# Performance work log

Measured on AMD Instinct MI355X. Metric: run time of the kernel, lower is better.

The kernel has to match this reference:

```python
import jax, jax.numpy as jnp
import numpy as np

B, S, D = 4, 2048, 1024
H, DH = 16, 64

def setup_inputs() -> dict:
    key = jax.random.key(0)
    kx, kq, kk, kv, ko = jax.random.split(key, 5)
    scale = 1.0 / np.sqrt(D)
    return {
        "x": jax.random.normal(kx, (B, S, D), dtype=jnp.float32),
        "Wq": jax.random.normal(kq, (D, H * DH), dtype=jnp.float32) * scale,
        "Wk": jax.random.normal(kk, (D, H * DH), dtype=jnp.float32) * scale,
        "Wv": jax.random.normal(kv, (D, H * DH), dtype=jnp.float32) * scale,
        "Wo": jax.random.normal(ko, (H * DH, D), dtype=jnp.float32) * scale,
    }

def reference(x, Wq, Wk, Wv, Wo):
    b, s, _ = x.shape
    # projections -> [b, h, s, dh]
    q = (x @ Wq).reshape(b, s, H, DH).transpose(0, 2, 1, 3)
    k = (x @ Wk).reshape(b, s, H, DH).transpose(0, 2, 1, 3)
    v = (x @ Wv).reshape(b, s, H, DH).transpose(0, 2, 1, 3)
    logits = jnp.einsum("bhqd,bhkd->bhqk", q, k) / jnp.sqrt(jnp.float32(DH))
    # mask = triu(ones, diagonal=1): True above diagonal -> masked
    mask = jnp.triu(jnp.ones((s, s), dtype=bool), k=1)
    logits = jnp.where(mask, -jnp.inf, logits)
    probs = jax.nn.softmax(logits, axis=-1)
    attn = jnp.einsum("bhqk,bhkd->bhqd", probs, v)
    attn = attn.transpose(0, 2, 1, 3).reshape(b, s, H * DH)
    return attn @ Wo
```

## Files before the change

### kernel.cpp

```cpp
#include <hip/hip_runtime.h>
#include <stdint.h>

#define NB 4
#define NS 2048
#define ND 1024
#define NH 16
#define NDH 64

typedef __attribute__((ext_vector_type(8))) short bf16x8;
typedef __attribute__((ext_vector_type(4))) float f32x4;
typedef __attribute__((ext_vector_type(2))) unsigned int u32x2;

#define MFMA16(a, b, c) __builtin_amdgcn_mfma_f32_16x16x32_bf16((a), (b), (c), 0, 0, 0)

__device__ __forceinline__ uint16_t f2bf(float f) {
  uint32_t u = __builtin_bit_cast(uint32_t, f);
  return (uint16_t)((u + 0x7FFFu + ((u >> 16) & 1u)) >> 16);
}

__device__ __forceinline__ uint32_t pk2(float lo, float hi) {
  return (__builtin_bit_cast(uint32_t, hi) & 0xFFFF0000u) |
         (__builtin_bit_cast(uint32_t, lo) >> 16);
}

__device__ __forceinline__ void gload_lds16(const void* g, void* l) {
  __builtin_amdgcn_global_load_lds(
      (const __attribute__((address_space(1))) uint32_t*)(uintptr_t)g,
      (__attribute__((address_space(3))) uint32_t*)(uintptr_t)l, 16, 0, 0);
}

__global__ __launch_bounds__(256) void prep_kernel(const float* __restrict__ x,
                                                   const float* __restrict__ Wq,
                                                   const float* __restrict__ Wk,
                                                   const float* __restrict__ Wv,
                                                   const float* __restrict__ Wo,
                                                   uint16_t* __restrict__ xb,
                                                   uint16_t* __restrict__ Wt3,
                                                   uint16_t* __restrict__ Wot) {
  const int bid = blockIdx.x;
  if (bid < 4096) {
    __shared__ uint16_t tile[32][33];
    const int which = bid >> 10;
    const int tl = bid & 1023;
    const int bx = (tl & 31) * 32;
    const int by = (tl >> 5) * 32;
    const int tx = threadIdx.x & 31;
    const int ty = threadIdx.x >> 5;
    const float* W = (which == 0) ? Wq : (which == 1) ? Wk : (which == 2) ? Wv : Wo;
    uint16_t* Wt = (which < 3) ? (Wt3 + (size_t)which * (1u << 20)) : Wot;
#pragma unroll
    for (int j = 0; j < 4; j++)
      tile[ty + j * 8][tx] = f2bf(W[(size_t)(by + ty + j * 8) * 1024 + bx + tx]);
    __syncthreads();
#pragma unroll
    for (int j = 0; j < 4; j++)
      Wt[(size_t)(bx + ty + j * 8) * 1024 + by + tx] = tile[tx][ty + j * 8];
  } else {
    const int i = (bid - 4096) * 256 + threadIdx.x;
    const float4 f = *(const float4*)(x + (size_t)i * 4);
    union { uint16_t u[4]; uint64_t q; } o;
    o.u[0] = f2bf(f.x); o.u[1] = f2bf(f.y); o.u[2] = f2bf(f.z); o.u[3] = f2bf(f.w);
    *(uint64_t*)(xb + (size_t)i * 4) = o.q;
  }
}

template <int MODE, int NBX>
__global__ __launch_bounds__(256) void gemm_bt(const uint16_t* __restrict__ A,
                                               const uint16_t* __restrict__ Bt,
                                               uint16_t* __restrict__ O0,
                                               uint16_t* __restrict__ O1,
                                               uint16_t* __restrict__ O2,
                                               float* __restrict__ OF) {
  __shared__ uint16_t lds[2][2][128 * 64];
  const int tid = threadIdx.x;
  const int lane = tid & 63;
  const int wave = tid >> 6;
  const int wr = wave >> 1, wc = wave & 1;
  const int l15 = lane & 15, lg = lane >> 4;

  const int nwg = NBX * 64;
  const int wg = ((int)blockIdx.x & 7) * (nwg >> 3) + ((int)blockIdx.x >> 3);
  const int st = wg >> 5, in32 = wg & 31;
  const int sy = in32 >> 2, sx = in32 & 3;
  const int stx = st % (NBX / 4), sty = st / (NBX / 4);
  const int row0 = (sty * 8 + sy) * 128;
  const int col0 = (stx * 4 + sx) * 128;

  f32x4 acc[4][4];
#pragma unroll
  for (int i = 0; i < 4; i++)
#pragma unroll
    for (int j = 0; j < 4; j++) acc[i][j] = f32x4{0.f, 0.f, 0.f, 0.f};

  const char* Ag = (const char*)A + (size_t)row0 * 2048;
  const char* Bg = (const char*)Bt + (size_t)col0 * 2048;

  const int srr = tid >> 3;
  const int csrc = ((tid & 7) - srr) & 7;

#define STAGE_TILE(buf, t)                                                          \
  {                                                                                 \
    char* la = (char*)&lds[buf][0][0] + wave * 1024;                                \
    char* lb = (char*)&lds[buf][1][0] + wave * 1024;                                \
    _Pragma("unroll") for (int j = 0; j < 4; ++j) {                                 \
      const size_t off = (size_t)(j * 32 + srr) * 2048 + (size_t)(t) * 128 + csrc * 16; \
      gload_lds16(Ag + off, la + j * 4096);                                         \
      gload_lds16(Bg + off, lb + j * 4096);                                         \
    }                                                                               \
  }

  STAGE_TILE(0, 0);
  __syncthreads();

  int cur = 0;
  for (int t = 0; t < 16; ++t) {
    if (t < 15) STAGE_TILE(cur ^ 1, t + 1);
    const char* cA = (const char*)&lds[cur][0][0];
    const char* cB = (const char*)&lds[cur][1][0];
    bf16x8 af[4][2], bfr[4][2];
#pragma unroll
    for (int mi = 0; mi < 4; mi++) {
      const int row = wr * 64 + mi * 16 + l15;
#pragma unroll
      for (int ks = 0; ks < 2; ks++) {
        const int ch = (ks * 4 + lg + (l15 & 7)) & 7;
        af[mi][ks] = *(const bf16x8*)(cA + row * 128 + ch * 16);
      }
    }
#pragma unroll
    for (int ni = 0; ni < 4; ni++) {
      const int row = wc * 64 + ni * 16 + l15;
#pragma unroll
      for (int ks = 0; ks < 2; ks++) {
        const int ch = (ks * 4 + lg + (l15 & 7)) & 7;
        bfr[ni][ks] = *(const bf16x8*)(cB + row * 128 + ch * 16);
      }
    }
#pragma unroll
    for (int ks = 0; ks < 2; ks++)
#pragma unroll
      for (int mi = 0; mi < 4; mi++)
#pragma unroll
        for (int ni = 0; ni < 4; ni++)
          acc[mi][ni] = MFMA16(af[mi][ks], bfr[ni][ks], acc[mi][ni]);
    __syncthreads();
    cur ^= 1;
  }

#pragma unroll
  for (int mi = 0; mi < 4; mi++) {
#pragma unroll
    for (int ni = 0; ni < 4; ni++) {
      const int c = col0 + wc * 64 + ni * 16 + l15;
      const int rbase = row0 + wr * 64 + mi * 16 + lg * 4;
#pragma unroll
      for (int i = 0; i < 4; i++) {
        const int r = rbase + i;
        const float v = acc[mi][ni][i];
        if (MODE == 0) {
          const int which = c >> 10, cc = c & 1023;
          const int h = cc >> 6, dh = cc & 63;
          const int b = r >> 11, s = r & 2047;
          const size_t hb = (size_t)(b * NH + h);
          if (which == 0)
            O0[(hb * NS + s) * 64 + dh] = f2bf(v * 0.18033688011112042f);
          else if (which == 1)
            O1[(hb * NS + s) * 64 + dh] = f2bf(v);
          else
            O2[(((hb * 32 + (s >> 6)) * 64 + dh) * 64) + (s & 63)] = f2bf(v);
        } else {
          OF[(size_t)r * 1024 + c] = v;
        }
      }
    }
  }
#undef STAGE_TILE
}

__device__ __forceinline__ void stage_kv(const char* __restrict__ Kg,
                                         const char* __restrict__ Vg,
                                         char* kl, char* vl, int lane) {
#pragma unroll
  for (int j = 0; j < 8; ++j) {
    const int y = j * 1024 + lane * 16;
    const int r = y >> 7;
    const int zs = (r << 7) | ((((y >> 4) - r) & 7) << 4);
    gload_lds16(Kg + zs, kl + j * 1024);
    gload_lds16(Vg + zs, vl + j * 1024);
  }
}

__device__ __forceinline__ void attn_unit(const uint16_t* __restrict__ Qh,
                                          const char* __restrict__ Kg,
                                          const char* __restrict__ Vg,
                                          uint16_t* __restrict__ Aout,
                                          int b, int h, int gp, int l15, int lg, int lane,
                                          char* kl, char* vl,
                                          uint16_t (*pX)[64][16]) {
  const int qbA = gp * 32;
  const int qbB = qbA + 16;
  const int tmax = gp >> 1;
  const int nfdA = (2 * gp) & 3;
  const int nfdB = nfdA + 1;

  stage_kv(Kg, Vg, kl, vl, lane);

  const bf16x8 qfA0 = *(const bf16x8*)&Qh[(size_t)(qbA + l15) * 64 + lg * 8];
  const bf16x8 qfA1 = *(const bf16x8*)&Qh[(size_t)(qbA + l15) * 64 + 32 + lg * 8];
  const bf16x8 qfB0 = *(const bf16x8*)&Qh[(size_t)(qbB + l15) * 64 + lg * 8];
  const bf16x8 qfB1 = *(const bf16x8*)&Qh[(size_t)(qbB + l15) * 64 + 32 + lg * 8];

  const short one_bf = (short)0x3F80;
  const bf16x8 ones = {one_bf, one_bf, one_bf, one_bf, one_bf, one_bf, one_bf, one_bf};

  const int rsw = l15 & 7;

  const int wcol = ((lg + (l15 >> 2)) & 3) * 4;
  const int rr = l15 >> 2, cc0 = l15 & 3;
  const int rot = (2 * lg) & 3;
  const uint32_t pb = (uint32_t)(uintptr_t)&pX[0][0][0];
  const uint32_t addr0 = pb + (uint32_t)(lg * 256 + rr * 32 + (((cc0 + rot) & 3) * 8));
  const uint32_t addr1 = pb + (uint32_t)(lg * 256 + 128 + rr * 32 + (((cc0 + rot + 1) & 3) * 8));

  f32x4 oA[4], oB[4];
  f32x4 rsA = f32x4{0.f, 0.f, 0.f, 0.f};
  f32x4 rsB = f32x4{0.f, 0.f, 0.f, 0.f};
#pragma unroll
  for (int i = 0; i < 4; i++) {
    oA[i] = f32x4{0.f, 0.f, 0.f, 0.f};
    oB[i] = f32x4{0.f, 0.f, 0.f, 0.f};
  }

  for (int t = 0; t <= tmax; ++t) {
    asm volatile("s_waitcnt vmcnt(0)" ::: "memory");
    bf16x8 kf[4][2], vf[4][2];
#pragma unroll
    for (int nf = 0; nf < 4; ++nf)
#pragma unroll
      for (int kk = 0; kk < 2; ++kk) {
        const int off = (nf * 16 + l15) * 128 + (((kk * 4 + lg) + rsw) & 7) * 16;
        kf[nf][kk] = *(const bf16x8*)(kl + off);
        vf[nf][kk] = *(const bf16x8*)(vl + off);
      }
    asm volatile("s_waitcnt lgkmcnt(0)" ::: "memory");
    if (t < tmax) stage_kv(Kg + (size_t)(t + 1) * 8192, Vg + (size_t)(t + 1) * 8192, kl, vl, lane);

    const int nfmA = (t == tmax) ? nfdA : 3;
    const int nfmB = (t == tmax) ? nfdB : 3;
#pragma unroll
    for (int nf = 0; nf < 4; ++nf) {
      if (nf <= nfmB) {
        f32x4 a = f32x4{0.f, 0.f, 0.f, 0.f};
        a = MFMA16(qfB0, kf[nf][0], a);
        a = MFMA16(qfB1, kf[nf][1], a);
        if (t == tmax && nf == nfdB) {
#pragma unroll
          for (int i = 0; i < 4; i++)
            if (l15 > lg * 4 + i) a[i] = -1e30f;
        }
        {
          const float e0 = exp2f(a[0]), e1 = exp2f(a[1]);
          const float e2 = exp2f(a[2]), e3 = exp2f(a[3]);
          *(uint64_t*)&pX[1][nf * 16 + l15][wcol] =
              ((uint64_t)pk2(e2, e3) << 32) | pk2(e0, e1);
        }
        if (nf <= nfmA) {
          f32x4 c = f32x4{0.f, 0.f, 0.f, 0.f};
          c = MFMA16(qfA0, kf[nf][0], c);
          c = MFMA16(qfA1, kf[nf][1], c);
          if (t == tmax && nf == nfdA) {
#pragma unroll
            for (int i = 0; i < 4; i++)
              if (l15 > lg * 4 + i) c[i] = -1e30f;
          }
          const float e0 = exp2f(c[0]), e1 = exp2f(c[1]);
          const float e2 = exp2f(c[2]), e3 = exp2f(c[3]);
          *(uint64_t*)&pX[0][nf * 16 + l15][wcol] =
              ((uint64_t)pk2(e2, e3) << 32) | pk2(e0, e1);
        } else {
          *(uint64_t*)&pX[0][nf * 16 + l15][wcol] = 0ull;
        }
      } else {
        *(uint64_t*)&pX[0][nf * 16 + l15][wcol] = 0ull;
        *(uint64_t*)&pX[1][nf * 16 + l15][wcol] = 0ull;
      }
    }
    u32x2 a0, a1, a2, a3, b0, b1, b2, b3;
    asm volatile(
        "ds_read_b64_tr_b16 %0, %8\n\t"
        "ds_read_b64_tr_b16 %1, %9\n\t"
        "ds_read_b64_tr_b16 %2, %8 offset:1024\n\t"
        "ds_read_b64_tr_b16 %3, %9 offset:1024\n\t"
        "ds_read_b64_tr_b16 %4, %8 offset:2048\n\t"
        "ds_read_b64_tr_b16 %5, %9 offset:2048\n\t"
        "ds_read_b64_tr_b16 %6, %8 offset:3072\n\t"
        "ds_read_b64_tr_b16 %7, %9 offset:3072\n\t"
        "s_waitcnt lgkmcnt(0)"
        : "=&v"(a0), "=&v"(a1), "=&v"(a2), "=&v"(a3),
          "=&v"(b0), "=&v"(b1), "=&v"(b2), "=&v"(b3)
        : "v"(addr0), "v"(addr1)
        : "memory");
    union { u32x2 u2[2]; bf16x8 v8; } uA0, uA1, uB0, uB1;
    uA0.u2[0] = a0; uA0.u2[1] = a1;
    uA1.u2[0] = a2; uA1.u2[1] = a3;
    uB0.u2[0] = b0; uB0.u2[1] = b1;
    uB1.u2[0] = b2; uB1.u2[1] = b3;
    const bf16x8 paA0 = uA0.v8, paA1 = uA1.v8;
    const bf16x8 paB0 = uB0.v8, paB1 = uB1.v8;
    rsA = MFMA16(paA0, ones, rsA);
    rsA = MFMA16(paA1, ones, rsA);
    rsB = MFMA16(paB0, ones, rsB);
    rsB = MFMA16(paB1, ones, rsB);
#pragma unroll
    for (int df = 0; df < 4; ++df) {
      oA[df] = MFMA16(paA0, vf[df][0], oA[df]);
      oA[df] = MFMA16(paA1, vf[df][1], oA[df]);
      oB[df] = MFMA16(paB0, vf[df][0], oB[df]);
      oB[df] = MFMA16(paB1, vf[df][1], oB[df]);
    }
  }

#pragma unroll
  for (int df = 0; df < 4; ++df) {
#pragma unroll
    for (int i = 0; i < 4; i++) {
      const int qA = qbA + lg * 4 + i;
      const int qB = qbB + lg * 4 + i;
      Aout[((size_t)(b * NS + qA)) * 1024 + h * 64 + df * 16 + l15] = f2bf(oA[df][i] / rsA[i]);
      Aout[((size_t)(b * NS + qB)) * 1024 + h * 64 + df * 16 + l15] = f2bf(oB[df][i] / rsB[i]);
    }
  }
}

__global__ __launch_bounds__(256) void attn_fwd(const uint16_t* __restrict__ Q,
                                                const uint16_t* __restrict__ K,
                                                const uint16_t* __restrict__ Vt,
                                                uint16_t* __restrict__ Aout) {
  const int bid = blockIdx.x;
  const int xcd = bid & 7;
  const int sp = (bid >> 3) & 3;
  const int gblk = bid >> 5;

  const int w = threadIdx.x >> 6;
  const int lane = threadIdx.x & 63;
  const int l15 = lane & 15, lg = lane >> 4;
  const int g = gblk * 4 + w;

  __shared__ __align__(16) uint16_t plds[4][2][64][16];
  __shared__ __align__(16) char kstage[4][8192];
  __shared__ __align__(16) char vstage[4][8192];

  for (int seg = 0; seg < 2; ++seg) {
    const int slot = sp * 2 + seg;
    const int bh = (slot << 3) | xcd;
    const int gp = seg ? (63 - g) : g;
    const uint16_t* Qh = Q + (size_t)bh * (NS * 64);
    const char* Kg = (const char*)(K + (size_t)bh * (NS * 64));
    const char* Vg = (const char*)(Vt + (size_t)bh * (32 * 64 * 64));
    attn_unit(Qh, Kg, Vg, Aout, bh >> 4, bh & 15, gp, l15, lg, lane,
              kstage[w], vstage[w], plds[w]);
  }
}

extern "C" void kernel_launch(void* const* d_in, const int* in_sizes, int n_in,
                              void* d_out, int out_size, void* d_ws, size_t ws_size,
                              hipStream_t stream) {
  const float* x = (const float*)d_in[0];
  const float* Wq = (const float*)d_in[1];
  const float* Wk = (const float*)d_in[2];
  const float* Wv = (const float*)d_in[3];
  const float* Wo = (const float*)d_in[4];
  float* out = (float*)d_out;

  char* ws = (char*)d_ws;
  uint16_t* xb = (uint16_t*)(ws);
  uint16_t* Wt3 = (uint16_t*)(ws + (16u << 20));
  uint16_t* Wot = (uint16_t*)(ws + (22u << 20));
  uint16_t* Qb = (uint16_t*)(ws + (24u << 20));
  uint16_t* Kb = (uint16_t*)(ws + (40u << 20));
  uint16_t* Vt = (uint16_t*)(ws + (56u << 20));
  uint16_t* attn = xb;

  prep_kernel<<<12288, 256, 0, stream>>>(x, Wq, Wk, Wv, Wo, xb, Wt3, Wot);

  gemm_bt<0, 24><<<1536, 256, 0, stream>>>(xb, Wt3, Qb, Kb, Vt, nullptr);
  attn_fwd<<<512, 256, 0, stream>>>(Qb, Kb, Vt, attn);
  gemm_bt<1, 8><<<512, 256, 0, stream>>>(attn, Wot, nullptr, nullptr, nullptr, out);
}
```

Before: 185.0 us.

## Share K/V staging across warps in a block with cooperative loads

Each block now handles four adjacent 32-row query groups of the same batch-head. The four warps load each K/V tile into one shared LDS buffer cooperatively instead of each warp staging its own copy. This removes redundant global-to-LDS traffic and cuts LDS usage, which may allow higher occupancy. In exchange it adds two block-wide barriers per tile, and warps with shorter causal ranges sit idle while later tiles are staged for the others.

```diff
diff --git a/kernel.cpp b/kernel.cpp
--- a/kernel.cpp
+++ b/kernel.cpp
@@ -177,33 +177,37 @@
 #undef STAGE_TILE
 }
 
-__device__ __forceinline__ void stage_kv(const char* __restrict__ Kg,
-                                         const char* __restrict__ Vg,
-                                         char* kl, char* vl, int lane) {
-#pragma unroll
-  for (int j = 0; j < 8; ++j) {
-    const int y = j * 1024 + lane * 16;
+__device__ __forceinline__ void stage_kv_coop(const char* __restrict__ Kg,
+                                              const char* __restrict__ Vg,
+                                              char* kl, char* vl, int w, int lane) {
+#pragma unroll
+  for (int j = 0; j < 2; ++j) {
+    const int c = w + j * 4;
+    const int y = c * 1024 + lane * 16;
     const int r = y >> 7;
     const int zs = (r << 7) | ((((y >> 4) - r) & 7) << 4);
-    gload_lds16(Kg + zs, kl + j * 1024);
-    gload_lds16(Vg + zs, vl + j * 1024);
-  }
-}
-
-__device__ __forceinline__ void attn_unit(const uint16_t* __restrict__ Qh,
-                                          const char* __restrict__ Kg,
-                                          const char* __restrict__ Vg,
-                                          uint16_t* __restrict__ Aout,
-                                          int b, int h, int gp, int l15, int lg, int lane,
-                                          char* kl, char* vl,
-                                          uint16_t (*pX)[64][16]) {
+    gload_lds16(Kg + zs, kl + c * 1024);
+    gload_lds16(Vg + zs, vl + c * 1024);
+  }
+}
+
+__device__ __forceinline__ void attn_strip(const uint16_t* __restrict__ Qh,
+                                           const char* __restrict__ Kg,
+                                           const char* __restrict__ Vg,
+                                           uint16_t* __restrict__ Aout,
+                                           int b, int h, int u, int w,
+                                           int l15, int lg, int lane,
+                                           char* kl, char* vl,
+                                           uint16_t (*pX)[64][16]) {
+  const int gp = 4 * u + w;
+  const int ntiles = 2 * u + 2;
+  const int tmaxw = gp >> 1;
+  const int nfdA = (2 * w) & 3;
+  const int nfdB = nfdA + 1;
   const int qbA = gp * 32;
   const int qbB = qbA + 16;
-  const int tmax = gp >> 1;
-  const int nfdA = (2 * gp) & 3;
-  const int nfdB = nfdA + 1;
-
-  stage_kv(Kg, Vg, kl, vl, lane);
+
+  stage_kv_coop(Kg, Vg, kl, vl, w, lane);
 
   const bf16x8 qfA0 = *(const bf16x8*)&Qh[(size_t)(qbA + l15) * 64 + lg * 8];
   const bf16x8 qfA1 = *(const bf16x8*)&Qh[(size_t)(qbA + l15) * 64 + 32 + lg * 8];
@@ -214,7 +218,6 @@
   const bf16x8 ones = {one_bf, one_bf, one_bf, one_bf, one_bf, one_bf, one_bf, one_bf};
 
   const int rsw = l15 & 7;
-
   const int wcol = ((lg + (l15 >> 2)) & 3) * 4;
   const int rr = l15 >> 2, cc0 = l15 & 3;
   const int rot = (2 * lg) & 3;
@@ -231,29 +234,35 @@
     oB[i] = f32x4{0.f, 0.f, 0.f, 0.f};
   }
 
-  for (int t = 0; t <= tmax; ++t) {
-    asm volatile("s_waitcnt vmcnt(0)" ::: "memory");
+  for (int t = 0; t < ntiles; ++t) {
+    __syncthreads();
+    const bool active = (t <= tmaxw);
     bf16x8 kf[4][2], vf[4][2];
-#pragma unroll
-    for (int nf = 0; nf < 4; ++nf)
-#pragma unroll
-      for (int kk = 0; kk < 2; ++kk) {
-        const int off = (nf * 16 + l15) * 128 + (((kk * 4 + lg) + rsw) & 7) * 16;
-        kf[nf][kk] = *(const bf16x8*)(kl + off);
-        vf[nf][kk] = *(const bf16x8*)(vl + off);
-      }
-    asm volatile("s_waitcnt lgkmcnt(0)" ::: "memory");
-    if (t < tmax) stage_kv(Kg + (size_t)(t + 1) * 8192, Vg + (size_t)(t + 1) * 8192, kl, vl, lane);
-
-    const int nfmA = (t == tmax) ? nfdA : 3;
-    const int nfmB = (t == tmax) ? nfdB : 3;
+    if (active) {
+#pragma unroll
+      for (int nf = 0; nf < 4; ++nf)
+#pragma unroll
+        for (int kk = 0; kk < 2; ++kk) {
+          const int off = (nf * 16 + l15) * 128 + (((kk * 4 + lg) + rsw) & 7) * 16;
+          kf[nf][kk] = *(const bf16x8*)(kl + off);
+          vf[nf][kk] = *(const bf16x8*)(vl + off);
+        }
+    }
+    __syncthreads();
+    if (t + 1 < ntiles)
+      stage_kv_coop(Kg + (size_t)(t + 1) * 8192, Vg + (size_t)(t + 1) * 8192, kl, vl, w, lane);
+    if (!active) continue;
+
+    const bool last = (t == tmaxw);
+    const int nfmA = last ? nfdA : 3;
+    const int nfmB = last ? nfdB : 3;
 #pragma unroll
     for (int nf = 0; nf < 4; ++nf) {
       if (nf <= nfmB) {
         f32x4 a = f32x4{0.f, 0.f, 0.f, 0.f};
         a = MFMA16(qfB0, kf[nf][0], a);
         a = MFMA16(qfB1, kf[nf][1], a);
-        if (t == tmax && nf == nfdB) {
+        if (last && nf == nfdB) {
 #pragma unroll
           for (int i = 0; i < 4; i++)
             if (l15 > lg * 4 + i) a[i] = -1e30f;
@@ -268,7 +277,7 @@
           f32x4 c = f32x4{0.f, 0.f, 0.f, 0.f};
           c = MFMA16(qfA0, kf[nf][0], c);
           c = MFMA16(qfA1, kf[nf][1], c);
-          if (t == tmax && nf == nfdA) {
+          if (last && nf == nfdA) {
 #pragma unroll
             for (int i = 0; i < 4; i++)
               if (l15 > lg * 4 + i) c[i] = -1e30f;
@@ -338,27 +347,26 @@
                                                 uint16_t* __restrict__ Aout) {
   const int bid = blockIdx.x;
   const int xcd = bid & 7;
-  const int sp = (bid >> 3) & 3;
-  const int gblk = bid >> 5;
+  const int slot = (bid >> 3) & 7;
+  const int sp = bid >> 6;
+  const int bh = (slot << 3) | xcd;
 
   const int w = threadIdx.x >> 6;
   const int lane = threadIdx.x & 63;
   const int l15 = lane & 15, lg = lane >> 4;
-  const int g = gblk * 4 + w;
 
   __shared__ __align__(16) uint16_t plds[4][2][64][16];
-  __shared__ __align__(16) char kstage[4][8192];
-  __shared__ __align__(16) char vstage[4][8192];
+  __shared__ __align__(16) char kstage[8192];
+  __shared__ __align__(16) char vstage[8192];
+
+  const uint16_t* Qh = Q + (size_t)bh * (NS * 64);
+  const char* Kg = (const char*)(K + (size_t)bh * (NS * 64));
+  const char* Vg = (const char*)(Vt + (size_t)bh * (32 * 64 * 64));
+  const int b = bh >> 4, h = bh & 15;
 
   for (int seg = 0; seg < 2; ++seg) {
-    const int slot = sp * 2 + seg;
-    const int bh = (slot << 3) | xcd;
-    const int gp = seg ? (63 - g) : g;
-    const uint16_t* Qh = Q + (size_t)bh * (NS * 64);
-    const char* Kg = (const char*)(K + (size_t)bh * (NS * 64));
-    const char* Vg = (const char*)(Vt + (size_t)bh * (32 * 64 * 64));
-    attn_unit(Qh, Kg, Vg, Aout, bh >> 4, bh & 15, gp, l15, lg, lane,
-              kstage[w], vstage[w], plds[w]);
+    const int u = seg ? (15 - sp) : sp;
+    attn_strip(Qh, Kg, Vg, Aout, b, h, u, w, l15, lg, lane, kstage, vstage, plds[w]);
   }
 }
 
```

New measurement: 192.5 us. 1.04x slower.
